# Performance work log

Hardware: AMD Instinct MI355X
Metric: run time of the kernel (lower is better)

Reference implementation:

```python
import jax, jax.numpy as jnp
import numpy as np
from jax import lax

B, S, E = 256, 2048, 128
H = 64   # LSTM hidden
H2 = 2   # head hidden
K = 13   # number of RNN heads


def setup_inputs() -> dict:
    key = jax.random.key(0)
    ks = jax.random.split(key, 12)
    u = lambda k, shape, bound: jax.random.uniform(k, shape, jnp.float32, -bound, bound)
    kl = 1.0 / np.sqrt(H)
    kh = 1.0 / np.sqrt(H2)
    inp = {
        "input": jax.random.normal(ks[0], (B, S, E), jnp.float32),
        "lengths": jax.random.randint(ks[1], (B,), 1, S + 1).astype(jnp.int64),
        # LSTM params (PyTorch layout: gates ordered i,f,g,o)
        "lstm_Wih": u(ks[2], (4 * H, E), kl),
        "lstm_Whh": u(ks[3], (4 * H, H), kl),
        "lstm_bih": u(ks[4], (4 * H,), kl),
        "lstm_bhh": u(ks[5], (4 * H,), kl),
        # 13 stacked tanh-RNN heads
        "head_Wih": u(ks[6], (K, H2, H), kh),
        "head_Whh": u(ks[7], (K, H2, H2), kh),
        "head_bih": u(ks[8], (K, H2), kh),
        "head_bhh": u(ks[9], (K, H2), kh),
    }
    return inp


def _forward(input, lengths, lstm_Wih, lstm_Whh, lstm_bih, lstm_bhh,
             head_Wih, head_Whh, head_bih, head_bhh):
    b, s, _ = input.shape

    def step(carry, xt):
        h, c, hk = carry                      # h:[B,H] c:[B,H] hk:[K,B,H2]
        g = xt @ lstm_Wih.T + lstm_bih + h @ lstm_Whh.T + lstm_bhh  # [B,4H]
        i, f, gg, o = jnp.split(g, 4, axis=-1)
        c = jax.nn.sigmoid(f) * c + jax.nn.sigmoid(i) * jnp.tanh(gg)
        h = jax.nn.sigmoid(o) * jnp.tanh(c)
        # 13 tiny tanh-RNN heads fed by the LSTM output at this timestep
        z = (jnp.einsum('bf,kof->kbo', h, head_Wih) + head_bih[:, None, :]
             + jnp.einsum('kbp,kop->kbo', hk, head_Whh) + head_bhh[:, None, :])
        hk = jnp.tanh(z)
        return (h, c, hk), hk

    init = (jnp.zeros((b, H), input.dtype), jnp.zeros((b, H), input.dtype),
            jnp.zeros((K, b, H2), input.dtype))
    xs = jnp.swapaxes(input, 0, 1)            # [S,B,E]
    _, ys = lax.scan(step, init, xs)          # ys: [S,K,B,H2]

    # gather each head's output at the last valid timestep (lengths-1), then sigmoid
    idx = lengths.astype(jnp.int32) - 1       # [B]
    last = ys[idx, :, jnp.arange(b), :]       # [B,K,H2]
    return jax.nn.sigmoid(jnp.swapaxes(last, 0, 1))  # [K,B,H2] = [13,B,2]


def reference(input, lengths, lstm_Wih, lstm_Whh, lstm_bih, lstm_bhh,
              head_Wih, head_Whh, head_bih, head_bhh):
    return _forward(input, lengths, lstm_Wih, lstm_Whh, lstm_bih, lstm_bhh,
                    head_Wih, head_Whh, head_bih, head_bhh)
```

## Files before the change

### kernel.cpp

```cpp
#include <hip/hip_runtime.h>
#include <cstddef>
#include <cstdint>


namespace {

constexpr int B_ = 256, S_ = 2048, E_ = 128, H_ = 64, G_ = 256, H2_ = 2;

typedef short short8 __attribute__((ext_vector_type(8)));
typedef float f4 __attribute__((ext_vector_type(4)));

__device__ __forceinline__ float sigm(float x) {
    return __builtin_amdgcn_rcpf(1.0f + __expf(-x));
}
__device__ __forceinline__ float tanh_fast(float x) {
    return 1.0f - 2.0f * __builtin_amdgcn_rcpf(1.0f + __expf(2.0f * x));
}
__device__ __forceinline__ float dot4(float4 a, float4 b) {
    return a.x * b.x + a.y * b.y + a.z * b.z + a.w * b.w;
}
__device__ __forceinline__ short f2bf(float f) {
    union { float f; uint32_t u; } a; a.f = f;
    uint32_t r = a.u + 0x7FFFu + ((a.u >> 16) & 1u);
    return (short)(r >> 16);
}
__device__ __forceinline__ float bf2f(short s) {
    union { uint32_t u; float f; } a; a.u = ((uint32_t)(uint16_t)s) << 16;
    return a.f;
}
__device__ __forceinline__ void cvt8(float4 a, float4 b, short8& hi, short8& lo) {
    float v[8] = {a.x, a.y, a.z, a.w, b.x, b.y, b.z, b.w};
    #pragma unroll
    for (int i = 0; i < 8; ++i) {
        short h = f2bf(v[i]);
        hi[i] = h;
        lo[i] = f2bf(v[i] - bf2f(h));
    }
}
#define PIN4(v) asm volatile("" : "+v"(v.x), "+v"(v.y), "+v"(v.z), "+v"(v.w))

__global__ __launch_bounds__(256) void k1_gemm(
    const float* __restrict__ x, const int* __restrict__ lengths,
    const float* __restrict__ Wih, const float* __restrict__ bih,
    const float* __restrict__ bhh, float* __restrict__ gx, int cs, int tcLog)
{
    const int Tc = 1 << tcLog;
    const int t = threadIdx.x;
    const int lane = t & 63, wv = t >> 6;
    const int lm = lane & 15, quad = lane >> 4;
    const int nbase = blockIdx.y * 128 + wv * 32;
    const int rowblk = blockIdx.x * 128;

    short8 Bh[2][4], Bl[2][4];
    float bias[2];
    #pragma unroll
    for (int nt = 0; nt < 2; ++nt) {
        const int n = nbase + nt * 16 + lm;
        bias[nt] = bih[n] + bhh[n];
        #pragma unroll
        for (int kk = 0; kk < 4; ++kk) {
            const float4* wp = (const float4*)(Wih + n * E_ + kk * 32 + quad * 8);
            cvt8(wp[0], wp[1], Bh[nt][kk], Bl[nt][kk]);
        }
    }

    for (int slab = 0; slab < 8; ++slab) {
        const int row0 = rowblk + slab * 16;
        const int b = row0 >> tcLog;
        const int tb = row0 & (Tc - 1);
        int len = lengths[b]; len = len < 1 ? 1 : (len > S_ ? S_ : len);
        if (cs + tb >= len) continue;

        const float* xr = x + ((size_t)b * S_ + cs + tb + lm) * E_;
        short8 Ah[4], Al[4];
        #pragma unroll
        for (int kk = 0; kk < 4; ++kk) {
            const float4* ap = (const float4*)(xr + kk * 32 + quad * 8);
            cvt8(ap[0], ap[1], Ah[kk], Al[kk]);
        }
        f4 acc[2] = {{0,0,0,0},{0,0,0,0}};
        #pragma unroll
        for (int kk = 0; kk < 4; ++kk) {
            #pragma unroll
            for (int nt = 0; nt < 2; ++nt) {
                acc[nt] = __builtin_amdgcn_mfma_f32_16x16x32_bf16(Ah[kk], Bh[nt][kk], acc[nt], 0, 0, 0);
                acc[nt] = __builtin_amdgcn_mfma_f32_16x16x32_bf16(Al[kk], Bh[nt][kk], acc[nt], 0, 0, 0);
                acc[nt] = __builtin_amdgcn_mfma_f32_16x16x32_bf16(Ah[kk], Bl[nt][kk], acc[nt], 0, 0, 0);
            }
        }
        float* gp = gx + ((size_t)b * Tc + tb) * G_;
        #pragma unroll
        for (int nt = 0; nt < 2; ++nt) {
            #pragma unroll
            for (int r = 0; r < 4; ++r) {
                gp[(quad * 4 + r) * G_ + nbase + nt * 16 + lm] = acc[nt][r] + bias[nt];
            }
        }
    }
}

__global__ __launch_bounds__(320, 1) void k2_recur(
    const float* __restrict__ gx, const int* __restrict__ lengths,
    const float* __restrict__ Whh, const float* __restrict__ hWih,
    const float* __restrict__ hWhh, const float* __restrict__ hbih,
    const float* __restrict__ hbhh, float* __restrict__ out,
    float* __restrict__ stH, float* __restrict__ stC, float* __restrict__ stHK,
    int cs, int Tc)
{
    const int b = blockIdx.x, t = threadIdx.x;
    int len = lengths[b]; len = len < 1 ? 1 : (len > S_ ? S_ : len);
    if (cs > len) return;
    const int ce = cs + Tc;

    __shared__ __align__(16) float h_lds[2][H_];

    const bool isGate = t < 256;
    const int p = (t >> 2) & 63, q = t & 3;

    float4 wh[4][4];
    if (isGate) {
        #pragma unroll
        for (int k = 0; k < 4; ++k) {
            const int g = q ^ k;
            const float4* wp = (const float4*)(Whh + (g * 64 + p) * H_ + q * 16);
            #pragma unroll
            for (int i = 0; i < 4; ++i) wh[k][i] = wp[i];
        }
        #pragma unroll
        for (int k = 0; k < 4; ++k) {
            #pragma unroll
            for (int i = 0; i < 4; ++i) PIN4(wh[k][i]);
        }
    }

    const int th = t - 256;
    const bool isHead = (t >= 256) && (th < 52);
    const int ko = (th >> 1) & 31, half = th & 1;
    const int hk_k = ko >> 1, hk_o = ko & 1;
    float4 wk[8] = {};
    float hb = 0.f, w0 = 0.f, w1 = 0.f;
    if (isHead) {
        const int r = hk_k * 2 + hk_o;
        const float4* kp = (const float4*)(hWih + r * H_ + half * 32);
        #pragma unroll
        for (int i = 0; i < 8; ++i) wk[i] = kp[i];
        hb = hbih[r] + hbhh[r];
        w0 = hWhh[r * 2 + 0];
        w1 = hWhh[r * 2 + 1];
        #pragma unroll
        for (int i = 0; i < 8; ++i) PIN4(wk[i]);
    }

    float c = 0.f, hk = 0.f;
    if (cs == 0) {
        if (t < 64) h_lds[0][t] = 0.f;
    } else {
        if (t < 64) h_lds[cs & 1][t] = stH[b * 64 + t];
        if (isGate && q == 0) c = stC[b * 64 + p];
        if (isHead && half == 0) hk = stHK[b * 32 + ko];
    }
    __syncthreads();

    const float* gxp = gx + (size_t)b * Tc * G_ + (q * 64 + p);
    float gxa = 0.f, gxb = 0.f;
    if (isGate) {
        if (cs < len) gxa = gxp[0];
        if (cs + 1 < len && cs + 1 < ce) gxb = gxp[G_];
    }

    auto headStep = [&](int u, const float* hbuf) {
        const float4* hv = (const float4*)(hbuf + half * 32);
        float ph = 0.f;
        #pragma unroll
        for (int i = 0; i < 8; ++i) ph += dot4(wk[i], hv[i]);
        ph += __shfl_xor(ph, 1);
        const float partner = __shfl_xor(hk, 2);
        if (half == 0) {
            const float h0 = (hk_o == 0) ? hk : partner;
            const float h1 = (hk_o == 0) ? partner : hk;
            hk = tanh_fast(ph + hb + w0 * h0 + w1 * h1);
            if (u == len) out[(hk_k * B_ + b) * H2_ + hk_o] = sigm(hk);
        }
    };

    for (int u = cs; u < ce; ++u) {
        const float* hbuf = h_lds[u & 1];
        if (u >= 1 && isHead) headStep(u, hbuf);
        if (u == len) return;

        if (isGate) {
            const float4* hv = (const float4*)(hbuf + q * 16);
            const float4 h0 = hv[0], h1 = hv[1], h2 = hv[2], h3 = hv[3];
            float P0 = dot4(wh[0][0], h0) + dot4(wh[0][1], h1) + dot4(wh[0][2], h2) + dot4(wh[0][3], h3);
            float P1 = dot4(wh[1][0], h0) + dot4(wh[1][1], h1) + dot4(wh[1][2], h2) + dot4(wh[1][3], h3);
            float P2 = dot4(wh[2][0], h0) + dot4(wh[2][1], h1) + dot4(wh[2][2], h2) + dot4(wh[2][3], h3);
            float P3 = dot4(wh[3][0], h0) + dot4(wh[3][1], h1) + dot4(wh[3][2], h2) + dot4(wh[3][3], h3);
            float a_  = P0 + __shfl_xor(P1, 1);
            float b2_ = P2 + __shfl_xor(P3, 1);
            float v   = a_ + __shfl_xor(b2_, 2) + gxa;
            const bool isg = (q == 2);
            const float s = sigm(isg ? 2.f * v : v);
            const float act = isg ? 2.f * s - 1.f : s;
            const float r1 = __shfl_xor(act, 1);
            const float r2 = __shfl_xor(act, 2);
            const float r3 = __shfl_xor(act, 3);
            if (q == 0) {
                c = r1 * c + act * r2;
                h_lds[(u + 1) & 1][p] = r3 * tanh_fast(c);
            }
            gxa = gxb;
            const int un = u + 2;
            gxb = (un < len && un < ce) ? gxp[(size_t)(un - cs) * G_] : 0.f;
        }
        __syncthreads();
    }

    if (t < 64) stH[b * 64 + t] = h_lds[ce & 1][t];
    if (isGate && q == 0) stC[b * 64 + p] = c;
    if (isHead && half == 0) stHK[b * 32 + ko] = hk;

    if (ce == S_ && len == S_) {
        if (isHead) headStep(S_, h_lds[S_ & 1]);
    }
}

}

extern "C" void kernel_launch(void* const* d_in, const int* in_sizes, int n_in,
                              void* d_out, int out_size, void* d_ws, size_t ws_size,
                              hipStream_t stream) {
    const float* x    = (const float*)d_in[0];
    const int*   len  = (const int*)d_in[1];
    const float* Wih  = (const float*)d_in[2];
    const float* Whh  = (const float*)d_in[3];
    const float* bih  = (const float*)d_in[4];
    const float* bhh  = (const float*)d_in[5];
    const float* hWih = (const float*)d_in[6];
    const float* hWhh = (const float*)d_in[7];
    const float* hbih = (const float*)d_in[8];
    const float* hbhh = (const float*)d_in[9];
    float* out = (float*)d_out;

    int tcLog = 8;
    while (tcLog > 5) {
        size_t need = (size_t)B_ * ((size_t)1 << tcLog) * G_ * 4 + 160 * 1024;
        if (need <= ws_size) break;
        --tcLog;
    }
    const int Tc = 1 << tcLog;
    float* gxbuf = (float*)d_ws;
    size_t gxBytes = (size_t)B_ * Tc * G_ * 4;
    float* stH  = (float*)((char*)d_ws + gxBytes);
    float* stC  = stH + B_ * 64;
    float* stHK = stC + B_ * 64;

    for (int cs = 0; cs < S_; cs += Tc) {
        dim3 g1(B_ * Tc / 128, 2);
        hipLaunchKernelGGL(k1_gemm, g1, dim3(256), 0, stream,
                           x, len, Wih, bih, bhh, gxbuf, cs, tcLog);
        hipLaunchKernelGGL(k2_recur, dim3(B_), dim3(320), 0, stream,
                           gxbuf, len, Whh, hWih, hWhh, hbih, hbhh, out,
                           stH, stC, stHK, cs, Tc);
    }
}
```

Baseline: 2.096 ms.

## Run LSTM recurrence as a single wavefront with per-lane full gate dot products

```diff
diff --git a/kernel.cpp b/kernel.cpp
--- a/kernel.cpp
+++ b/kernel.cpp
@@ -9,6 +9,7 @@
 
 typedef short short8 __attribute__((ext_vector_type(8)));
 typedef float f4 __attribute__((ext_vector_type(4)));
+typedef float f2 __attribute__((ext_vector_type(2)));
 
 __device__ __forceinline__ float sigm(float x) {
     return __builtin_amdgcn_rcpf(1.0f + __expf(-x));
@@ -37,7 +38,6 @@
         lo[i] = f2bf(v[i] - bf2f(h));
     }
 }
-#define PIN4(v) asm volatile("" : "+v"(v.x), "+v"(v.y), "+v"(v.z), "+v"(v.w))
 
 __global__ __launch_bounds__(256) void k1_gemm(
     const float* __restrict__ x, const int* __restrict__ lengths,
@@ -99,7 +99,7 @@
     }
 }
 
-__global__ __launch_bounds__(320, 1) void k2_recur(
+__global__ __launch_bounds__(64, 1) void k2_recur(
     const float* __restrict__ gx, const int* __restrict__ lengths,
     const float* __restrict__ Whh, const float* __restrict__ hWih,
     const float* __restrict__ hWhh, const float* __restrict__ hbih,
@@ -107,120 +107,127 @@
     float* __restrict__ stH, float* __restrict__ stC, float* __restrict__ stHK,
     int cs, int Tc)
 {
-    const int b = blockIdx.x, t = threadIdx.x;
+    const int b = blockIdx.x, p = threadIdx.x;
     int len = lengths[b]; len = len < 1 ? 1 : (len > S_ ? S_ : len);
     if (cs > len) return;
     const int ce = cs + Tc;
 
-    __shared__ __align__(16) float h_lds[2][H_];
-
-    const bool isGate = t < 256;
-    const int p = (t >> 2) & 63, q = t & 3;
-
-    float4 wh[4][4];
-    if (isGate) {
-        #pragma unroll
-        for (int k = 0; k < 4; ++k) {
-            const int g = q ^ k;
-            const float4* wp = (const float4*)(Whh + (g * 64 + p) * H_ + q * 16);
-            #pragma unroll
-            for (int i = 0; i < 4; ++i) wh[k][i] = wp[i];
-        }
-        #pragma unroll
-        for (int k = 0; k < 4; ++k) {
-            #pragma unroll
-            for (int i = 0; i < 4; ++i) PIN4(wh[k][i]);
-        }
-    }
-
-    const int th = t - 256;
-    const bool isHead = (t >= 256) && (th < 52);
-    const int ko = (th >> 1) & 31, half = th & 1;
-    const int hk_k = ko >> 1, hk_o = ko & 1;
-    float4 wk[8] = {};
+    __shared__ __align__(16) float hbuf[2][H_];
+
+    f2 w2[4][32];
+    #pragma unroll
+    for (int g = 0; g < 4; ++g) {
+        const f2* wp = (const f2*)(Whh + (size_t)(g * 64 + p) * H_);
+        #pragma unroll
+        for (int ch = 0; ch < 32; ++ch) w2[g][ch] = wp[ch];
+    }
+
+    const bool isHead = p < 26;
+    f2 wk2[32];
     float hb = 0.f, w0 = 0.f, w1 = 0.f;
     if (isHead) {
-        const int r = hk_k * 2 + hk_o;
-        const float4* kp = (const float4*)(hWih + r * H_ + half * 32);
-        #pragma unroll
-        for (int i = 0; i < 8; ++i) wk[i] = kp[i];
-        hb = hbih[r] + hbhh[r];
-        w0 = hWhh[r * 2 + 0];
-        w1 = hWhh[r * 2 + 1];
-        #pragma unroll
-        for (int i = 0; i < 8; ++i) PIN4(wk[i]);
-    }
-
-    float c = 0.f, hk = 0.f;
+        const f2* kp = (const f2*)(hWih + (size_t)p * H_);
+        #pragma unroll
+        for (int ch = 0; ch < 32; ++ch) wk2[ch] = kp[ch];
+        hb = hbih[p] + hbhh[p];
+        w0 = hWhh[p * 2 + 0];
+        w1 = hWhh[p * 2 + 1];
+    } else {
+        #pragma unroll
+        for (int ch = 0; ch < 32; ++ch) wk2[ch] = (f2){0.f, 0.f};
+    }
+
+    float c = 0.f, h = 0.f, hk = 0.f;
     if (cs == 0) {
-        if (t < 64) h_lds[0][t] = 0.f;
+        hbuf[0][p] = 0.f;
     } else {
-        if (t < 64) h_lds[cs & 1][t] = stH[b * 64 + t];
-        if (isGate && q == 0) c = stC[b * 64 + p];
-        if (isHead && half == 0) hk = stHK[b * 32 + ko];
-    }
-    __syncthreads();
-
-    const float* gxp = gx + (size_t)b * Tc * G_ + (q * 64 + p);
-    float gxa = 0.f, gxb = 0.f;
-    if (isGate) {
-        if (cs < len) gxa = gxp[0];
-        if (cs + 1 < len && cs + 1 < ce) gxb = gxp[G_];
-    }
-
-    auto headStep = [&](int u, const float* hbuf) {
-        const float4* hv = (const float4*)(hbuf + half * 32);
-        float ph = 0.f;
-        #pragma unroll
-        for (int i = 0; i < 8; ++i) ph += dot4(wk[i], hv[i]);
-        ph += __shfl_xor(ph, 1);
-        const float partner = __shfl_xor(hk, 2);
-        if (half == 0) {
-            const float h0 = (hk_o == 0) ? hk : partner;
-            const float h1 = (hk_o == 0) ? partner : hk;
-            hk = tanh_fast(ph + hb + w0 * h0 + w1 * h1);
-            if (u == len) out[(hk_k * B_ + b) * H2_ + hk_o] = sigm(hk);
-        }
-    };
+        h = stH[b * 64 + p];
+        c = stC[b * 64 + p];
+        if (isHead) hk = stHK[b * 26 + p];
+        hbuf[cs & 1][p] = h;
+    }
+
+    const float* gxp = gx + (size_t)b * Tc * G_ + p;
+    float ga0 = 0.f, ga1 = 0.f, ga2 = 0.f, ga3 = 0.f;
+    float gb0 = 0.f, gb1 = 0.f, gb2 = 0.f, gb3 = 0.f;
+    if (cs < len) {
+        ga0 = gxp[0]; ga1 = gxp[64]; ga2 = gxp[128]; ga3 = gxp[192];
+    }
+    if (cs + 1 < len && cs + 1 < ce) {
+        const float* r = gxp + G_;
+        gb0 = r[0]; gb1 = r[64]; gb2 = r[128]; gb3 = r[192];
+    }
 
     for (int u = cs; u < ce; ++u) {
-        const float* hbuf = h_lds[u & 1];
-        if (u >= 1 && isHead) headStep(u, hbuf);
-        if (u == len) return;
-
-        if (isGate) {
-            const float4* hv = (const float4*)(hbuf + q * 16);
-            const float4 h0 = hv[0], h1 = hv[1], h2 = hv[2], h3 = hv[3];
-            float P0 = dot4(wh[0][0], h0) + dot4(wh[0][1], h1) + dot4(wh[0][2], h2) + dot4(wh[0][3], h3);
-            float P1 = dot4(wh[1][0], h0) + dot4(wh[1][1], h1) + dot4(wh[1][2], h2) + dot4(wh[1][3], h3);
-            float P2 = dot4(wh[2][0], h0) + dot4(wh[2][1], h1) + dot4(wh[2][2], h2) + dot4(wh[2][3], h3);
-            float P3 = dot4(wh[3][0], h0) + dot4(wh[3][1], h1) + dot4(wh[3][2], h2) + dot4(wh[3][3], h3);
-            float a_  = P0 + __shfl_xor(P1, 1);
-            float b2_ = P2 + __shfl_xor(P3, 1);
-            float v   = a_ + __shfl_xor(b2_, 2) + gxa;
-            const bool isg = (q == 2);
-            const float s = sigm(isg ? 2.f * v : v);
-            const float act = isg ? 2.f * s - 1.f : s;
-            const float r1 = __shfl_xor(act, 1);
-            const float r2 = __shfl_xor(act, 2);
-            const float r3 = __shfl_xor(act, 3);
-            if (q == 0) {
-                c = r1 * c + act * r2;
-                h_lds[(u + 1) & 1][p] = r3 * tanh_fast(c);
+        const float* hrow = hbuf[u & 1];
+        f2 a0 = {0.f, 0.f}, a1 = {0.f, 0.f}, a2 = {0.f, 0.f}, a3 = {0.f, 0.f};
+        f2 ak = {0.f, 0.f};
+        #pragma unroll
+        for (int q4 = 0; q4 < 16; ++q4) {
+            const float4 hv = *(const float4*)(hrow + q4 * 4);
+            const f2 hA = {hv.x, hv.y};
+            const f2 hB = {hv.z, hv.w};
+            a0 = __builtin_elementwise_fma(w2[0][q4 * 2],     hA, a0);
+            a1 = __builtin_elementwise_fma(w2[1][q4 * 2],     hA, a1);
+            a2 = __builtin_elementwise_fma(w2[2][q4 * 2],     hA, a2);
+            a3 = __builtin_elementwise_fma(w2[3][q4 * 2],     hA, a3);
+            ak = __builtin_elementwise_fma(wk2[q4 * 2],       hA, ak);
+            a0 = __builtin_elementwise_fma(w2[0][q4 * 2 + 1], hB, a0);
+            a1 = __builtin_elementwise_fma(w2[1][q4 * 2 + 1], hB, a1);
+            a2 = __builtin_elementwise_fma(w2[2][q4 * 2 + 1], hB, a2);
+            a3 = __builtin_elementwise_fma(w2[3][q4 * 2 + 1], hB, a3);
+            ak = __builtin_elementwise_fma(wk2[q4 * 2 + 1],   hB, ak);
+        }
+
+        if (u >= 1) {
+            const float ah = ak[0] + ak[1] + hb;
+            const float partner = __shfl_xor(hk, 1);
+            const float h0 = (p & 1) ? partner : hk;
+            const float h1 = (p & 1) ? hk : partner;
+            const float hkn = tanh_fast(ah + w0 * h0 + w1 * h1);
+            if (isHead) hk = hkn;
+            if (u == len) {
+                if (isHead) out[((p >> 1) * B_ + b) * H2_ + (p & 1)] = sigm(hk);
+                return;
             }
-            gxa = gxb;
-            const int un = u + 2;
-            gxb = (un < len && un < ce) ? gxp[(size_t)(un - cs) * G_] : 0.f;
-        }
-        __syncthreads();
-    }
-
-    if (t < 64) stH[b * 64 + t] = h_lds[ce & 1][t];
-    if (isGate && q == 0) stC[b * 64 + p] = c;
-    if (isHead && half == 0) stHK[b * 32 + ko] = hk;
+        }
+
+        const float vi = a0[0] + a0[1] + ga0;
+        const float vf = a1[0] + a1[1] + ga1;
+        const float vg = a2[0] + a2[1] + ga2;
+        const float vo = a3[0] + a3[1] + ga3;
+        c = sigm(vf) * c + sigm(vi) * tanh_fast(vg);
+        h = sigm(vo) * tanh_fast(c);
+        hbuf[(u + 1) & 1][p] = h;
+
+        ga0 = gb0; ga1 = gb1; ga2 = gb2; ga3 = gb3;
+        const int un = u + 2;
+        if (un < len && un < ce) {
+            const float* r = gxp + (size_t)(un - cs) * G_;
+            gb0 = r[0]; gb1 = r[64]; gb2 = r[128]; gb3 = r[192];
+        } else {
+            gb0 = gb1 = gb2 = gb3 = 0.f;
+        }
+    }
+
+    stH[b * 64 + p] = h;
+    stC[b * 64 + p] = c;
+    if (isHead) stHK[b * 26 + p] = hk;
 
     if (ce == S_ && len == S_) {
-        if (isHead) headStep(S_, h_lds[S_ & 1]);
+        const float* hrow = hbuf[S_ & 1];
+        f2 ak = {0.f, 0.f};
+        #pragma unroll
+        for (int ch = 0; ch < 32; ++ch) {
+            const f2 hA = *(const f2*)(hrow + ch * 2);
+            ak = __builtin_elementwise_fma(wk2[ch], hA, ak);
+        }
+        const float ah = ak[0] + ak[1] + hb;
+        const float partner = __shfl_xor(hk, 1);
+        const float h0 = (p & 1) ? partner : hk;
+        const float h1 = (p & 1) ? hk : partner;
+        const float hkn = tanh_fast(ah + w0 * h0 + w1 * h1);
+        if (isHead) out[((p >> 1) * B_ + b) * H2_ + (p & 1)] = sigm(hkn);
     }
 }
 
@@ -258,7 +265,7 @@
         dim3 g1(B_ * Tc / 128, 2);
         hipLaunchKernelGGL(k1_gemm, g1, dim3(256), 0, stream,
                            x, len, Wih, bih, bhh, gxbuf, cs, tcLog);
-        hipLaunchKernelGGL(k2_recur, dim3(B_), dim3(320), 0, stream,
+        hipLaunchKernelGGL(k2_recur, dim3(B_), dim3(64), 0, stream,
                            gxbuf, len, Whh, hWih, hWhh, hbih, hbhh, out,
                            stH, stC, stHK, cs, Tc);
     }
```

New measurement: 3.024 ms. +44.2%, slower.
